# Kernel optimization log

Measured on AMD Instinct MI355X. Metric: run time of the kernel, lower is better.

The kernel has to match this reference:

```python
import jax, jax.numpy as jnp
from jax import lax
import numpy as np

SR = 16000
N_FFT = 400
HOP = 160
WIN = 400
N_MELS = 64
N_MFCC = 20
SMOOTH = 0.98


def _hann(n):
    # periodic Hann window (torch.hann_window default)
    return (0.5 - 0.5 * np.cos(2.0 * np.pi * np.arange(n) / n)).astype(np.float32)


def _mel_fbanks(n_freqs, n_mels, sr):
    # torchaudio melscale_fbanks: htk scale, norm=None, f_min=0, f_max=sr/2
    f_max = sr / 2.0
    all_freqs = np.linspace(0.0, f_max, n_freqs)
    m_max = 2595.0 * np.log10(1.0 + f_max / 700.0)
    m_pts = np.linspace(0.0, m_max, n_mels + 2)
    f_pts = 700.0 * (10.0 ** (m_pts / 2595.0) - 1.0)
    f_diff = np.diff(f_pts)                      # (n_mels+1,)
    slopes = f_pts[None, :] - all_freqs[:, None]  # (n_freqs, n_mels+2)
    down = -slopes[:, :-2] / f_diff[:-1]
    up = slopes[:, 2:] / f_diff[1:]
    fb = np.maximum(0.0, np.minimum(down, up))
    return fb.astype(np.float32)                 # (n_freqs, n_mels)


def _dct_mat(n_mfcc, n_mels):
    # torchaudio create_dct, norm='ortho'; returns (n_mels, n_mfcc)
    n = np.arange(n_mels)
    k = np.arange(n_mfcc)[:, None]
    dct = np.cos(np.pi / n_mels * (n[None, :] + 0.5) * k)  # (n_mfcc, n_mels)
    dct *= np.sqrt(2.0 / n_mels)
    dct[0] *= 1.0 / np.sqrt(2.0)
    return dct.T.astype(np.float32)


_WIN = jnp.asarray(_hann(WIN))
_FB = jnp.asarray(_mel_fbanks(N_FFT // 2 + 1, N_MELS, SR))
_DCT = jnp.asarray(_dct_mat(N_MFCC, N_MELS))


def _mel_power(wav):
    # center=True, reflect pad, power=2.0 -> mel spectrogram [B, n_mels, T]
    pad = N_FFT // 2
    x = jnp.pad(wav, ((0, 0), (pad, pad)), mode='reflect')
    n_frames = 1 + (x.shape[-1] - N_FFT) // HOP
    idx = HOP * jnp.arange(n_frames)[:, None] + jnp.arange(N_FFT)[None, :]
    frames = x[:, idx] * _WIN                       # [B, T, n_fft]
    spec = jnp.abs(jnp.fft.rfft(frames, axis=-1)) ** 2  # [B, T, n_freqs]
    return jnp.einsum('btf,fm->bmt', spec, _FB)     # [B, n_mels, T]


def _ema(mel, s):
    # per-timestep EMA smoothing (the original python loop) via lax.scan
    def step(prev, x):
        prev = s * prev + (1.0 - s) * x
        return prev, prev
    init = jnp.zeros(mel.shape[:-1], mel.dtype)
    _, sm = lax.scan(step, init, jnp.moveaxis(mel, -1, 0))
    return jnp.moveaxis(sm, 0, -1)


def setup_inputs() -> dict:
    key = jax.random.key(0)
    wav = jax.random.normal(key, (64, 160000), dtype=jnp.float32)
    return {'wav': wav}


def reference(wav):
    mel = _mel_power(wav)                 # [B, 64, T]
    sm = _ema(mel, SMOOTH)
    mel_norm = jnp.log1p(mel / (sm + 1e-6))
    # MFCC: 10*log10(clamp(mel, 1e-10)) then ortho DCT-II, take 20 coeffs
    mel_db = 10.0 * jnp.log10(jnp.maximum(mel, 1e-10))
    mfcc = jnp.einsum('bmt,mk->bkt', mel_db, _DCT)  # [B, 20, T]
    return mel_norm, mfcc
```

## Files before the change

### kernel.cpp

```cpp
#include <hip/hip_runtime.h>

#define T_FRAMES 1001
#define MEL_STRIDE 1008
#define P_STRIDE 268

#define OFF_WIN 0
#define OFF_BG  1696
#define OFF_FBG 108192
#define OFF_DCT16 120000
#define OFF_MEL 13748128

typedef unsigned int u32;
typedef unsigned short u16;
typedef __attribute__((ext_vector_type(8))) short bf16x8;
typedef __attribute__((ext_vector_type(8))) _Float16 f16x8;
typedef __attribute__((ext_vector_type(4))) float f32x4;

__device__ __forceinline__ u16 f2bf(float f) {
  u32 u = __float_as_uint(f);
  u32 r = (u + 0x7FFFu + ((u >> 16) & 1u)) >> 16;
  return (u16)r;
}

__device__ __forceinline__ float bf2f(u32 h) {
  return __uint_as_float(h << 16);
}

__device__ __forceinline__ int reflect_idx(int g) {
  g = (g < 0) ? -g : g;
  g = (g >= 160000) ? (319998 - g) : g;
  return g;
}

__global__ __launch_bounds__(256) void k_init(float* __restrict__ ws) {
  float* win = ws + OFF_WIN;
  u16* bg = (u16*)(ws + OFF_BG);
  u16* fbg = (u16*)(ws + OFF_FBG);
  _Float16* dct16 = (_Float16*)(ws + OFF_DCT16);
  const float W = 6.28318530717958647692f / 400.0f;
  int tid = blockIdx.x * 256 + threadIdx.x;
  int stride = gridDim.x * 256;
  for (int i = tid; i < 416; i += stride)
    win[i] = (i < 400) ? (0.5f - 0.5f * cosf((float)i * W)) : 0.0f;
  for (int i = tid; i < 32 * 64; i += stride) {
    int k = i >> 6, m = i & 63;
    float v = 0.0f;
    if (k < 20) {
      v = cosf(3.14159265358979323846f / 64.0f * ((float)m + 0.5f) * (float)k) * sqrtf(2.0f / 64.0f);
      if (k == 0) v *= 0.70710678118654752440f;
    }
    dct16[i] = (_Float16)v;
  }
  for (int i = tid; i < 13 * 16384; i += stride) {
    int kt = i >> 14;
    int r = i & 16383;
    int g = r >> 9;
    int khalf = (r >> 7) & 3;
    int c15 = (r >> 3) & 15;
    int e = r & 7;
    int col = g * 16 + c15;
    int n = kt * 32 + khalf * 8 + e;
    int bin = ((col >> 5) << 4) | (col & 15);
    int type = (col >> 4) & 1;
    float v = 0.0f;
    if (n < 400 && bin <= 200) {
      float a = (float)((n * bin) % 400) * W;
      v = type ? -sinf(a) : cosf(a);
    }
    bg[i] = f2bf(v);
  }
  for (int i = tid; i < 64 * 264; i += stride) {
    int m = i / 264, f = i % 264;
    float v = 0.0f;
    if (f <= 200) {
      float freq = 40.0f * (float)f;
      float m_max = 2595.0f * log10f(1.0f + 8000.0f / 700.0f);
      float ms = m_max / 65.0f;
      float fp0 = 700.0f * (powf(10.0f, (float)(m)     * ms / 2595.0f) - 1.0f);
      float fp1 = 700.0f * (powf(10.0f, (float)(m + 1) * ms / 2595.0f) - 1.0f);
      float fp2 = 700.0f * (powf(10.0f, (float)(m + 2) * ms / 2595.0f) - 1.0f);
      float dn = (freq - fp0) / (fp1 - fp0);
      float up = (fp2 - freq) / (fp2 - fp1);
      v = fmaxf(0.0f, fminf(dn, up));
    }
    fbg[i] = f2bf(v);
  }
}

__global__ __launch_bounds__(512, 2) void k_gemm(const float* __restrict__ wav,
                                                 const float* __restrict__ ws,
                                                 u16* __restrict__ mel,
                                                 float* __restrict__ mfcc) {
  extern __shared__ char sm[];
  const char* Bg = (const char*)(ws + OFF_BG);
  const u16* FBg = (const u16*)(ws + OFF_FBG);
  const _Float16* DCTg = (const _Float16*)(ws + OFF_DCT16);
  const float* win = ws + OFF_WIN;
  int tid = threadIdx.x, wid = tid >> 6, lane = tid & 63;
  int bx = blockIdx.x, b = blockIdx.y;
  const float* wv = wav + (size_t)b * 160000;

  {
    int kq = tid & 3, rowq = tid >> 2;
    int frame = bx * 128 + rowq;
    bool fvalid = (frame <= 1000);
#pragma unroll 4
    for (int kt = 0; kt < 13; ++kt) {
      int n0 = kt * 32 + kq * 8;
      int g0 = frame * 160 + n0 - 200;
      float ax[8];
      if (fvalid) {
        if (g0 >= 0 && g0 + 7 < 160000) {
          float4 u = *(const float4*)&wv[g0];
          float4 v = *(const float4*)&wv[g0 + 4];
          ax[0] = u.x; ax[1] = u.y; ax[2] = u.z; ax[3] = u.w;
          ax[4] = v.x; ax[5] = v.y; ax[6] = v.z; ax[7] = v.w;
        } else {
#pragma unroll
          for (int e = 0; e < 8; ++e) ax[e] = wv[reflect_idx(g0 + e)];
        }
      } else {
#pragma unroll
        for (int e = 0; e < 8; ++e) ax[e] = 0.0f;
      }
      float4 w0 = *(const float4*)&win[n0];
      float4 w1 = *(const float4*)&win[n0 + 4];
      uint4 pk;
      pk.x = (u32)f2bf(ax[0] * w0.x) | ((u32)f2bf(ax[1] * w0.y) << 16);
      pk.y = (u32)f2bf(ax[2] * w0.z) | ((u32)f2bf(ax[3] * w0.w) << 16);
      pk.z = (u32)f2bf(ax[4] * w1.x) | ((u32)f2bf(ax[5] * w1.y) << 16);
      pk.w = (u32)f2bf(ax[6] * w1.z) | ((u32)f2bf(ax[7] * w1.w) << 16);
      *(uint4*)(sm + kt * 8192 + kq * 2048 + rowq * 16) = pk;
    }
  }
  __syncthreads();

  int NG = (wid < 5) ? 2 : 1;
  int GB = (wid < 5) ? wid * 2 : wid + 5;

  f32x4 acc[8][4];
  const f32x4 zf = {0.0f, 0.0f, 0.0f, 0.0f};
#pragma unroll
  for (int mi = 0; mi < 8; ++mi)
#pragma unroll
    for (int j = 0; j < 4; ++j) acc[mi][j] = zf;

#pragma unroll
  for (int kt = 0; kt < 13; ++kt) {
    bf16x8 bfr[4];
    bfr[0] = *(const bf16x8*)(Bg + kt * 32768 + (2 * GB) * 1024 + lane * 16);
    bfr[1] = *(const bf16x8*)(Bg + kt * 32768 + (2 * GB + 1) * 1024 + lane * 16);
    if (NG == 2) {
      bfr[2] = *(const bf16x8*)(Bg + kt * 32768 + (2 * GB + 2) * 1024 + lane * 16);
      bfr[3] = *(const bf16x8*)(Bg + kt * 32768 + (2 * GB + 3) * 1024 + lane * 16);
    }
#pragma unroll
    for (int mi = 0; mi < 8; ++mi) {
      bf16x8 af = *(const bf16x8*)(sm + kt * 8192 + (lane >> 4) * 2048 +
                                   (mi * 16 + (lane & 15)) * 16);
      acc[mi][0] = __builtin_amdgcn_mfma_f32_16x16x32_bf16(af, bfr[0], acc[mi][0], 0, 0, 0);
      acc[mi][1] = __builtin_amdgcn_mfma_f32_16x16x32_bf16(af, bfr[1], acc[mi][1], 0, 0, 0);
      if (NG == 2) {
        acc[mi][2] = __builtin_amdgcn_mfma_f32_16x16x32_bf16(af, bfr[2], acc[mi][2], 0, 0, 0);
        acc[mi][3] = __builtin_amdgcn_mfma_f32_16x16x32_bf16(af, bfr[3], acc[mi][3], 0, 0, 0);
      }
    }
  }
  __syncthreads();

  u16* P = (u16*)sm;
#pragma unroll
  for (int j = 0; j < 2; ++j) {
    if (j < NG) {
      int bin = (GB + j) * 16 + (lane & 15);
#pragma unroll
      for (int mi = 0; mi < 8; ++mi)
#pragma unroll
        for (int r = 0; r < 4; ++r) {
          int row = mi * 16 + (lane >> 4) * 4 + r;
          float re = acc[mi][2 * j][r], im = acc[mi][2 * j + 1][r];
          P[row * P_STRIDE + bin] = f2bf(re * re + im * im);
        }
    }
  }
  {
    u32* P32 = (u32*)sm;
    for (int i = tid; i < 3072; i += 512) {
      int row = i / 24, c = i - row * 24;
      P32[row * 134 + 104 + c] = 0;
    }
  }
  __syncthreads();

  f32x4 macc[4];
#pragma unroll
  for (int nf = 0; nf < 4; ++nf) macc[nf] = zf;
#pragma unroll
  for (int kt = 0; kt < 8; ++kt) {
    int krow = kt * 32 + (lane >> 4) * 8;
    bf16x8 pb = *(const bf16x8*)&P[(wid * 16 + (lane & 15)) * P_STRIDE + krow];
#pragma unroll
    for (int nf = 0; nf < 4; ++nf) {
      bf16x8 fa = *(const bf16x8*)&FBg[(nf * 16 + (lane & 15)) * 264 + krow];
      macc[nf] = __builtin_amdgcn_mfma_f32_16x16x32_bf16(fa, pb, macc[nf], 0, 0, 0);
    }
  }

  int t = bx * 128 + wid * 16 + (lane & 15);
  if (t <= 1000) {
#pragma unroll
    for (int nf = 0; nf < 4; ++nf)
#pragma unroll
      for (int r = 0; r < 4; ++r) {
        int m = nf * 16 + (lane >> 4) * 4 + r;
        mel[((size_t)b * 64 + m) * MEL_STRIDE + t] = f2bf(macc[nf][r]);
      }
  }

  _Float16* db = (_Float16*)(sm + 69632);
  {
    int tl = wid * 16 + (lane & 15);
#pragma unroll
    for (int nf = 0; nf < 4; ++nf)
#pragma unroll
      for (int r = 0; r < 4; ++r) {
        int m = nf * 16 + (lane >> 4) * 4 + r;
        float d = 10.0f * log10f(fmaxf(macc[nf][r], 1e-10f));
        db[tl * 72 + m] = (_Float16)d;
      }
    f32x4 mf0 = zf, mf1 = zf;
#pragma unroll
    for (int mkt = 0; mkt < 2; ++mkt) {
      int ms = mkt * 32 + (lane >> 4) * 8;
      f16x8 pb3 = *(const f16x8*)&db[(wid * 16 + (lane & 15)) * 72 + ms];
      f16x8 fa0 = *(const f16x8*)&DCTg[((lane & 15)) * 64 + ms];
      f16x8 fa1 = *(const f16x8*)&DCTg[(16 + (lane & 15)) * 64 + ms];
      mf0 = __builtin_amdgcn_mfma_f32_16x16x32_f16(fa0, pb3, mf0, 0, 0, 0);
      mf1 = __builtin_amdgcn_mfma_f32_16x16x32_f16(fa1, pb3, mf1, 0, 0, 0);
    }
    if (t <= 1000) {
#pragma unroll
      for (int r = 0; r < 4; ++r) {
        int k0 = (lane >> 4) * 4 + r;
        mfcc[((size_t)b * 20 + k0) * 1001 + t] = mf0[r];
        int k1 = 16 + (lane >> 4) * 4 + r;
        if (k1 < 20)
          mfcc[((size_t)b * 20 + k1) * 1001 + t] = mf1[r];
      }
    }
  }
}

__global__ __launch_bounds__(256) void k_ema(const u16* __restrict__ mel,
                                             float* __restrict__ outp) {
  int wid = threadIdx.x >> 6, lane = threadIdx.x & 63;
  int row = blockIdx.x * 4 + wid;
  const u16* src = mel + (size_t)row * MEL_STRIDE + lane * 16;

  float x[16];
  if (lane < 63) {
    uint4 v0 = *(const uint4*)&src[0];
    uint4 v1 = *(const uint4*)&src[8];
    x[0] = bf2f(v0.x & 0xFFFF);  x[1] = bf2f(v0.x >> 16);
    x[2] = bf2f(v0.y & 0xFFFF);  x[3] = bf2f(v0.y >> 16);
    x[4] = bf2f(v0.z & 0xFFFF);  x[5] = bf2f(v0.z >> 16);
    x[6] = bf2f(v0.w & 0xFFFF);  x[7] = bf2f(v0.w >> 16);
    x[8] = bf2f(v1.x & 0xFFFF);  x[9] = bf2f(v1.x >> 16);
    x[10] = bf2f(v1.y & 0xFFFF); x[11] = bf2f(v1.y >> 16);
    x[12] = bf2f(v1.z & 0xFFFF); x[13] = bf2f(v1.z >> 16);
    x[14] = bf2f(v1.w & 0xFFFF); x[15] = bf2f(v1.w >> 16);
#pragma unroll
    for (int i = 0; i < 16; ++i)
      if (lane * 16 + i > 1000) x[i] = 0.0f;
  } else {
#pragma unroll
    for (int i = 0; i < 16; ++i) x[i] = 0.0f;
  }

  float B = 0.0f;
#pragma unroll
  for (int i = 0; i < 16; ++i) B = fmaf(0.98f, B, 0.02f * x[i]);
  float A = 1.0f;
#pragma unroll
  for (int i = 0; i < 16; ++i) A *= 0.98f;

#pragma unroll
  for (int d = 1; d < 64; d <<= 1) {
    float Ap = __shfl_up(A, d, 64);
    float Bp = __shfl_up(B, d, 64);
    if (lane >= d) {
      B = fmaf(A, Bp, B);
      A = A * Ap;
    }
  }
  float s = __shfl_up(B, 1, 64);
  if (lane == 0) s = 0.0f;

  float* dst = outp + (size_t)row * 1001 + lane * 16;
#pragma unroll
  for (int i = 0; i < 16; ++i) {
    s = fmaf(0.98f, s, 0.02f * x[i]);
    if (lane * 16 + i <= 1000) dst[i] = log1pf(x[i] / (s + 1e-6f));
  }
}

extern "C" void kernel_launch(void* const* d_in, const int* in_sizes, int n_in,
                              void* d_out, int out_size, void* d_ws, size_t ws_size,
                              hipStream_t stream) {
  const float* wav = (const float*)d_in[0];
  float* out = (float*)d_out;
  float* ws = (float*)d_ws;
  u16* mel = (u16*)(ws + OFF_MEL);

  hipFuncSetAttribute(reinterpret_cast<const void*>(k_gemm),
                      hipFuncAttributeMaxDynamicSharedMemorySize, 106496);

  hipLaunchKernelGGL(k_init, dim3(256), dim3(256), 0, stream, ws);
  hipLaunchKernelGGL(k_gemm, dim3(8, 64), dim3(512), 106496, stream, wav, ws, mel,
                     out + 4100096);
  hipLaunchKernelGGL(k_ema, dim3(1024), dim3(256), 0, stream, mel, out);
}
```

Before: 85.72 us.

## Split fused DFT/mel GEMM kernel into separate DFT and post kernels via global power buffer

The single kernel that computed the DFT power spectrum, mel filterbank GEMM and MFCC DCT is split in two. The DFT kernel now writes the bf16 power spectrum to a global workspace buffer instead of shared memory, and a new post kernel reads it back for the mel and DCT MFMAs using much less LDS. This removes the block-wide syncs and lets the post stage run at higher occupancy. The cost is an extra launch and a global round trip of roughly 35 MB of power data.

Result: slower. 94.52 us (+10.3%).

```diff
diff --git a/kernel.cpp b/kernel.cpp
--- a/kernel.cpp
+++ b/kernel.cpp
@@ -2,13 +2,14 @@
 
 #define T_FRAMES 1001
 #define MEL_STRIDE 1008
-#define P_STRIDE 268
+#define PG_STRIDE 272
 
 #define OFF_WIN 0
 #define OFF_BG  1696
 #define OFF_FBG 108192
 #define OFF_DCT16 120000
-#define OFF_MEL 13748128
+#define OFF_PG  121100
+#define OFF_MEL 9034000
 
 typedef unsigned int u32;
 typedef unsigned short u16;
@@ -87,18 +88,16 @@
   }
 }
 
-__global__ __launch_bounds__(512, 2) void k_gemm(const float* __restrict__ wav,
-                                                 const float* __restrict__ ws,
-                                                 u16* __restrict__ mel,
-                                                 float* __restrict__ mfcc) {
+__global__ __launch_bounds__(512, 2) void k_dft(const float* __restrict__ wav,
+                                                const float* __restrict__ ws,
+                                                u16* __restrict__ Pg) {
   extern __shared__ char sm[];
   const char* Bg = (const char*)(ws + OFF_BG);
-  const u16* FBg = (const u16*)(ws + OFF_FBG);
-  const _Float16* DCTg = (const _Float16*)(ws + OFF_DCT16);
   const float* win = ws + OFF_WIN;
   int tid = threadIdx.x, wid = tid >> 6, lane = tid & 63;
   int bx = blockIdx.x, b = blockIdx.y;
   const float* wv = wav + (size_t)b * 160000;
+  u16* Pt = Pg + ((size_t)b * 1024 + bx * 128) * PG_STRIDE;
 
   {
     int kq = tid & 3, rowq = tid >> 2;
@@ -166,9 +165,7 @@
       }
     }
   }
-  __syncthreads();
-
-  u16* P = (u16*)sm;
+
 #pragma unroll
   for (int j = 0; j < 2; ++j) {
     if (j < NG) {
@@ -179,18 +176,30 @@
         for (int r = 0; r < 4; ++r) {
           int row = mi * 16 + (lane >> 4) * 4 + r;
           float re = acc[mi][2 * j][r], im = acc[mi][2 * j + 1][r];
-          P[row * P_STRIDE + bin] = f2bf(re * re + im * im);
+          Pt[row * PG_STRIDE + bin] = f2bf(re * re + im * im);
         }
     }
   }
   {
-    u32* P32 = (u32*)sm;
-    for (int i = tid; i < 3072; i += 512) {
-      int row = i / 24, c = i - row * 24;
-      P32[row * 134 + 104 + c] = 0;
-    }
-  }
-  __syncthreads();
+    u32* Pt32 = (u32*)Pt;
+    for (int i = tid; i < 128 * 28; i += 512) {
+      int row = i / 28, c = i - row * 28;
+      Pt32[row * (PG_STRIDE / 2) + 104 + c] = 0;
+    }
+  }
+}
+
+__global__ __launch_bounds__(512) void k_post(const float* __restrict__ ws,
+                                              const u16* __restrict__ Pg,
+                                              u16* __restrict__ mel,
+                                              float* __restrict__ mfcc) {
+  extern __shared__ char sm[];
+  const u16* FBg = (const u16*)(ws + OFF_FBG);
+  const _Float16* DCTg = (const _Float16*)(ws + OFF_DCT16);
+  int tid = threadIdx.x, wid = tid >> 6, lane = tid & 63;
+  int bx = blockIdx.x, b = blockIdx.y;
+  const u16* Pt = Pg + ((size_t)b * 1024 + bx * 128) * PG_STRIDE;
+  const f32x4 zf = {0.0f, 0.0f, 0.0f, 0.0f};
 
   f32x4 macc[4];
 #pragma unroll
@@ -198,7 +207,7 @@
 #pragma unroll
   for (int kt = 0; kt < 8; ++kt) {
     int krow = kt * 32 + (lane >> 4) * 8;
-    bf16x8 pb = *(const bf16x8*)&P[(wid * 16 + (lane & 15)) * P_STRIDE + krow];
+    bf16x8 pb = *(const bf16x8*)&Pt[(wid * 16 + (lane & 15)) * PG_STRIDE + krow];
 #pragma unroll
     for (int nf = 0; nf < 4; ++nf) {
       bf16x8 fa = *(const bf16x8*)&FBg[(nf * 16 + (lane & 15)) * 264 + krow];
@@ -217,7 +226,7 @@
       }
   }
 
-  _Float16* db = (_Float16*)(sm + 69632);
+  _Float16* db = (_Float16*)sm;
   {
     int tl = wid * 16 + (lane & 15);
 #pragma unroll
@@ -310,13 +319,17 @@
   const float* wav = (const float*)d_in[0];
   float* out = (float*)d_out;
   float* ws = (float*)d_ws;
+  u16* Pg = (u16*)(ws + OFF_PG);
   u16* mel = (u16*)(ws + OFF_MEL);
 
-  hipFuncSetAttribute(reinterpret_cast<const void*>(k_gemm),
+  hipFuncSetAttribute(reinterpret_cast<const void*>(k_dft),
                       hipFuncAttributeMaxDynamicSharedMemorySize, 106496);
+  hipFuncSetAttribute(reinterpret_cast<const void*>(k_post),
+                      hipFuncAttributeMaxDynamicSharedMemorySize, 18432);
 
   hipLaunchKernelGGL(k_init, dim3(256), dim3(256), 0, stream, ws);
-  hipLaunchKernelGGL(k_gemm, dim3(8, 64), dim3(512), 106496, stream, wav, ws, mel,
+  hipLaunchKernelGGL(k_dft, dim3(8, 64), dim3(512), 106496, stream, wav, ws, Pg);
+  hipLaunchKernelGGL(k_post, dim3(8, 64), dim3(512), 18432, stream, ws, Pg, mel,
                      out + 4100096);
   hipLaunchKernelGGL(k_ema, dim3(1024), dim3(256), 0, stream, mel, out);
 }
```
